# Kernel tuning notes

Measured on AMD Instinct MI355X. Metric: run time of the kernel, lower is better.

## Reference

```python
import jax, jax.numpy as jnp
import numpy as np

D_MODEL = 1024
NUM_HEADS = 16
HEAD_DIM = D_MODEL // NUM_HEADS
BATCH = 4
SEQ = 1024


def setup_inputs() -> dict:
    key = jax.random.key(0)
    ks = jax.random.split(key, 11)
    s = 1.0 / np.sqrt(D_MODEL)
    return {
        "query": jax.random.normal(ks[0], (BATCH, SEQ, D_MODEL), jnp.float32),
        "key_": jax.random.normal(ks[1], (BATCH, SEQ, D_MODEL), jnp.float32),
        "value": jax.random.normal(ks[2], (BATCH, SEQ, D_MODEL), jnp.float32),
        "Wq": jax.random.uniform(ks[3], (D_MODEL, D_MODEL), jnp.float32, -s, s),
        "bq": jax.random.uniform(ks[4], (D_MODEL,), jnp.float32, -s, s),
        "Wk": jax.random.uniform(ks[5], (D_MODEL, D_MODEL), jnp.float32, -s, s),
        "bk": jax.random.uniform(ks[6], (D_MODEL,), jnp.float32, -s, s),
        "Wv": jax.random.uniform(ks[7], (D_MODEL, D_MODEL), jnp.float32, -s, s),
        "bv": jax.random.uniform(ks[8], (D_MODEL,), jnp.float32, -s, s),
        "Wo": jax.random.uniform(ks[9], (D_MODEL, D_MODEL), jnp.float32, -s, s),
        "bo": jax.random.uniform(ks[10], (D_MODEL,), jnp.float32, -s, s),
    }


def reference(query, key_, value, Wq, bq, Wk, bk, Wv, bv, Wo, bo):
    B, S, _ = query.shape
    scale = 1.0 / np.sqrt(HEAD_DIM).astype(np.float32)
    # projections, then split heads: [B, H, S, Dh]
    Q = (query @ Wq.T + bq).reshape(B, S, NUM_HEADS, HEAD_DIM).transpose(0, 2, 1, 3)
    K = (key_ @ Wk.T + bk).reshape(B, S, NUM_HEADS, HEAD_DIM).transpose(0, 2, 1, 3)
    V = (value @ Wv.T + bv).reshape(B, S, NUM_HEADS, HEAD_DIM).transpose(0, 2, 1, 3)
    scores = jnp.einsum("bhqd,bhkd->bhqk", Q, K) * scale
    attention = jax.nn.softmax(scores, axis=-1)
    out = jnp.einsum("bhqk,bhkd->bhqd", attention, V)
    out = out.transpose(0, 2, 1, 3).reshape(B, S, D_MODEL)
    return out @ Wo.T + bo, attention
```

## Files before the change

kernel.cpp:

```cpp
#include <hip/hip_runtime.h>
#include <hip/hip_bf16.h>

#define NH 16
#define S 1024
#define DH 64
#define DM 1024
#define MTOK 4096

typedef __attribute__((ext_vector_type(8))) short bf16x8;
typedef __attribute__((ext_vector_type(4))) float f32x4;
typedef __attribute__((ext_vector_type(16))) float f32x16;
typedef __attribute__((ext_vector_type(8))) unsigned short u16x8;
typedef __attribute__((ext_vector_type(4))) unsigned short u16x4;

__device__ inline unsigned short f2bf(float x) {
  __hip_bfloat16 h = __float2bfloat16(x);
  return __builtin_bit_cast(unsigned short, h);
}

__device__ inline unsigned cvt_pk_bf16(float lo, float hi_) {
  unsigned r;
  asm("v_cvt_pk_bf16_f32 %0, %1, %2" : "=v"(r) : "v"(lo), "v"(hi_));
  return r;
}

__device__ inline void gload16(const void* g, void* lds) {
  __builtin_amdgcn_global_load_lds((const __attribute__((address_space(1))) void*)g,
                                   (__attribute__((address_space(3))) void*)lds, 16, 0, 0);
}

__global__ __launch_bounds__(256) void cvt_all(
    const float* __restrict__ q, const float* __restrict__ k, const float* __restrict__ v,
    const float* __restrict__ wq, const float* __restrict__ wk,
    const float* __restrict__ wv, const float* __restrict__ wo,
    unsigned short* __restrict__ xq, unsigned short* __restrict__ xk,
    unsigned short* __restrict__ xv, unsigned short* __restrict__ wqb,
    unsigned short* __restrict__ wkb, unsigned short* __restrict__ wvb,
    unsigned short* __restrict__ wob) {
  const int bid = blockIdx.x;
  const float* src;
  unsigned short* dst;
  int lb;
  if (bid < 6144) {
    const int r = bid >> 11;
    lb = bid & 2047;
    src = (r == 0) ? q : ((r == 1) ? k : v);
    dst = (r == 0) ? xq : ((r == 1) ? xk : xv);
  } else {
    const int r = (bid - 6144) >> 9;
    lb = (bid - 6144) & 511;
    src = (r == 0) ? wq : ((r == 1) ? wk : ((r == 2) ? wv : wo));
    dst = (r == 0) ? wqb : ((r == 1) ? wkb : ((r == 2) ? wvb : wob));
  }
  const int i = lb * 256 + threadIdx.x;
  const float4* s4 = (const float4*)(src + (size_t)i * 8);
  float4 v0 = s4[0], v1 = s4[1];
  u16x8 o;
  o[0] = f2bf(v0.x); o[1] = f2bf(v0.y); o[2] = f2bf(v0.z); o[3] = f2bf(v0.w);
  o[4] = f2bf(v1.x); o[5] = f2bf(v1.y); o[6] = f2bf(v1.z); o[7] = f2bf(v1.w);
  *(u16x8*)(dst + (size_t)i * 8) = o;
}

__device__ inline void gemm_core128(const unsigned short* __restrict__ X,
                                    const unsigned short* __restrict__ W,
                                    unsigned short* As, unsigned short* Bs,
                                    int m0, int n0, f32x4 acc[4][4]) {
  const int t = threadIdx.x, l = t & 63, w = t >> 6;
  const int wr = w >> 1, wc = w & 1, cl = l & 15, kg = l >> 4;
  const int row0 = w * 16 + (l >> 2);
  const int kcol = (l & 3) * 8;

  const unsigned short* ga0 = X + (size_t)(m0 + row0) * DM + kcol;
  const unsigned short* ga1 = ga0 + (size_t)64 * DM;
  const unsigned short* gb0 = W + (size_t)(n0 + row0) * DM + kcol;
  const unsigned short* gb1 = gb0 + (size_t)64 * DM;
  char* lA0 = (char*)As + w * 1024;
  char* lA1 = (char*)As + w * 1024 + 4096;
  char* lB0 = (char*)Bs + w * 1024;
  char* lB1 = (char*)Bs + w * 1024 + 4096;

  for (int kt = 0; kt < DM; kt += 32) {
    __syncthreads();
    gload16(ga0 + kt, lA0);
    gload16(ga1 + kt, lA1);
    gload16(gb0 + kt, lB0);
    gload16(gb1 + kt, lB1);
    __syncthreads();
    bf16x8 a[4], b[4];
#pragma unroll
    for (int m = 0; m < 4; ++m)
      a[m] = *(const bf16x8*)&As[(wr * 64 + m * 16 + cl) * 32 + kg * 8];
#pragma unroll
    for (int n = 0; n < 4; ++n)
      b[n] = *(const bf16x8*)&Bs[(wc * 64 + n * 16 + cl) * 32 + kg * 8];
#pragma unroll
    for (int m = 0; m < 4; ++m)
#pragma unroll
      for (int n = 0; n < 4; ++n)
        acc[m][n] = __builtin_amdgcn_mfma_f32_16x16x32_bf16(a[m], b[n], acc[m][n], 0, 0, 0);
  }
}

__device__ inline void gemm_core64(const unsigned short* __restrict__ X,
                                   const unsigned short* __restrict__ W,
                                   unsigned short* As, unsigned short* Bs,
                                   int m0, int n0, f32x4 acc[2][4]) {
  const int t = threadIdx.x, l = t & 63, w = t >> 6;
  const int i4 = l >> 2, c8 = (l & 3) * 8;
  const int wr = w >> 1, wc = w & 1, cl = l & 15, kg = l >> 4;

  const unsigned short* ga  = X + (size_t)(m0 + w * 16 + i4) * DM + c8;
  const unsigned short* gb0 = W + (size_t)(n0 + w * 32 + i4) * DM + c8;
  const unsigned short* gb1 = W + (size_t)(n0 + w * 32 + 16 + i4) * DM + c8;
  char* lA  = (char*)As + w * 1024;
  char* lB0 = (char*)Bs + w * 2048;
  char* lB1 = (char*)Bs + w * 2048 + 1024;

  for (int kt = 0; kt < DM; kt += 32) {
    __syncthreads();
    gload16(ga + kt, lA);
    gload16(gb0 + kt, lB0);
    gload16(gb1 + kt, lB1);
    __syncthreads();
    bf16x8 a[2], b[4];
#pragma unroll
    for (int i = 0; i < 2; ++i)
      a[i] = *(const bf16x8*)&As[(wr * 32 + i * 16 + cl) * 32 + kg * 8];
#pragma unroll
    for (int j = 0; j < 4; ++j)
      b[j] = *(const bf16x8*)&Bs[(wc * 64 + j * 16 + cl) * 32 + kg * 8];
#pragma unroll
    for (int i = 0; i < 2; ++i)
#pragma unroll
      for (int j = 0; j < 4; ++j)
        acc[i][j] = __builtin_amdgcn_mfma_f32_16x16x32_bf16(a[i], b[j], acc[i][j], 0, 0, 0);
  }
}

__global__ __launch_bounds__(256) void proj_gemm(
    const unsigned short* __restrict__ X0, const unsigned short* __restrict__ X1,
    const unsigned short* __restrict__ X2, const unsigned short* __restrict__ W0,
    const unsigned short* __restrict__ W1, const unsigned short* __restrict__ W2,
    const float* __restrict__ b0, const float* __restrict__ b1, const float* __restrict__ b2,
    unsigned short* __restrict__ Y0, unsigned short* __restrict__ Y1,
    unsigned short* __restrict__ Y2) {
  __shared__ unsigned short As[128 * 32];
  __shared__ unsigned short Bs[128 * 32];
  const int z = blockIdx.z;
  const unsigned short* X = (z == 0) ? X0 : ((z == 1) ? X1 : X2);
  const unsigned short* W = (z == 0) ? W0 : ((z == 1) ? W1 : W2);
  const float* bias = (z == 0) ? b0 : ((z == 1) ? b1 : b2);
  const int m0 = blockIdx.y * 128, n0 = blockIdx.x * 128;

  f32x4 acc[4][4] = {};
  gemm_core128(X, W, As, Bs, m0, n0, acc);

  const int l = threadIdx.x & 63, w = threadIdx.x >> 6;
  const int wr = w >> 1, wc = w & 1, cl = l & 15, kg = l >> 4;
#pragma unroll
  for (int i = 0; i < 4; ++i) {
#pragma unroll
    for (int j = 0; j < 4; ++j) {
      const int gn = n0 + wc * 64 + j * 16 + cl;
      const float bv = bias[gn];
      const int h_ = gn >> 6, d_ = gn & 63;
      if (z == 2) {
        const int gm0 = m0 + wr * 64 + i * 16 + kg * 4;
        const int b_ = gm0 >> 10, s0 = gm0 & 1023;
        u16x4 vv;
#pragma unroll
        for (int r = 0; r < 4; ++r) vv[r] = f2bf(acc[i][j][r] + bv);
        *(u16x4*)&Y2[((size_t)(b_ * NH + h_) * DH + d_) * S + s0] = vv;
      } else {
#pragma unroll
        for (int r = 0; r < 4; ++r) {
          const int gm = m0 + wr * 64 + i * 16 + kg * 4 + r;
          const int b_ = gm >> 10, s_ = gm & 1023;
          const float val = acc[i][j][r] + bv;
          if (z == 0) {
            Y0[((size_t)(b_ * NH + h_) * S + s_) * DH + d_] = f2bf(val);
          } else {
            Y1[((size_t)(b_ * NH + h_) * S + s_) * DH + d_] = f2bf(val * 0.125f);
          }
        }
      }
    }
  }
}

__global__ __launch_bounds__(256) void out_gemm(const unsigned short* __restrict__ X,
                                                const unsigned short* __restrict__ W,
                                                const float* __restrict__ bias,
                                                float* __restrict__ Y) {
  __shared__ unsigned short As[64 * 32];
  __shared__ unsigned short Bs[128 * 32];
  const int m0 = blockIdx.y * 64, n0 = blockIdx.x * 128;
  f32x4 acc[2][4] = {};
  gemm_core64(X, W, As, Bs, m0, n0, acc);
  const int l = threadIdx.x & 63, w = threadIdx.x >> 6;
  const int wr = w >> 1, wc = w & 1, cl = l & 15, kg = l >> 4;
#pragma unroll
  for (int i = 0; i < 2; ++i) {
#pragma unroll
    for (int j = 0; j < 4; ++j) {
      const int gn = n0 + wc * 64 + j * 16 + cl;
      const float bv = bias[gn];
#pragma unroll
      for (int r = 0; r < 4; ++r) {
        const int gm = m0 + wr * 32 + i * 16 + kg * 4 + r;
        Y[(size_t)gm * DM + gn] = acc[i][j][r] + bv;
      }
    }
  }
}

__global__ __launch_bounds__(512, 4) void attn_mfma(const unsigned short* __restrict__ Qh,
                                                    const unsigned short* __restrict__ Kh,
                                                    const unsigned short* __restrict__ Vt,
                                                    float* __restrict__ attn,
                                                    unsigned short* __restrict__ OutH) {
  __shared__ float sums[8][32];
  __shared__ float Olds[8 * 64 * 33];
  const int t = threadIdx.x, l = t & 63, w = t >> 6;
  const int lq = l & 31, hi = l >> 5;
  const int bh = blockIdx.y;
  const int q0 = blockIdx.x * 32;

  const unsigned short* kb = Kh + (size_t)bh * S * DH;
  const unsigned short* vb = Vt + (size_t)bh * DH * S;

  unsigned e_pk[4][8];
  float sum = 0.f;

  {
    const unsigned short* qp = Qh + ((size_t)bh * S + q0 + lq) * DH + hi * 8;
    bf16x8 qf0 = *(const bf16x8*)(qp);
    bf16x8 qf1 = *(const bf16x8*)(qp + 16);
    bf16x8 qf2 = *(const bf16x8*)(qp + 32);
    bf16x8 qf3 = *(const bf16x8*)(qp + 48);
#pragma unroll
    for (int kt = 0; kt < 4; ++kt) {
      const unsigned short* kp = kb + (size_t)(w * 128 + kt * 32 + lq) * DH + hi * 8;
      f32x16 acc = {};
      __builtin_amdgcn_s_setprio(1);
      acc = __builtin_amdgcn_mfma_f32_32x32x16_bf16(*(const bf16x8*)(kp),      qf0, acc, 0, 0, 0);
      acc = __builtin_amdgcn_mfma_f32_32x32x16_bf16(*(const bf16x8*)(kp + 16), qf1, acc, 0, 0, 0);
      acc = __builtin_amdgcn_mfma_f32_32x32x16_bf16(*(const bf16x8*)(kp + 32), qf2, acc, 0, 0, 0);
      acc = __builtin_amdgcn_mfma_f32_32x32x16_bf16(*(const bf16x8*)(kp + 48), qf3, acc, 0, 0, 0);
      __builtin_amdgcn_s_setprio(0);
      float e[16];
#pragma unroll
      for (int r = 0; r < 16; ++r) e[r] = __expf(acc[r]);
#pragma unroll
      for (int r = 0; r < 16; ++r) sum += e[r];
#pragma unroll
      for (int j = 0; j < 8; ++j) e_pk[kt][j] = cvt_pk_bf16(e[2 * j], e[2 * j + 1]);
    }
  }
  sum += __shfl_xor(sum, 32);
  if (l < 32) sums[w][lq] = sum;
  __syncthreads();
  float tot = 0.f;
#pragma unroll
  for (int p = 0; p < 8; ++p) tot += sums[p][lq];
  const float inv = 1.0f / tot;

  f32x16 o0 = {}, o1 = {};
  float* ab = attn + ((size_t)bh << 20) + ((size_t)(q0 + lq) << 10) + w * 128;

#pragma unroll
  for (int kt = 0; kt < 4; ++kt) {
#pragma unroll
    for (int g = 0; g < 4; ++g) {
      const unsigned pk0 = e_pk[kt][2 * g], pk1 = e_pk[kt][2 * g + 1];
      f32x4 pv;
      pv[0] = __builtin_bit_cast(float, pk0 << 16) * inv;
      pv[1] = __builtin_bit_cast(float, pk0 & 0xffff0000u) * inv;
      pv[2] = __builtin_bit_cast(float, pk1 << 16) * inv;
      pv[3] = __builtin_bit_cast(float, pk1 & 0xffff0000u) * inv;
      *(f32x4*)(ab + kt * 32 + 8 * g + 4 * hi) = pv;
    }

    const unsigned wds0 = e_pk[kt][0], wds1 = e_pk[kt][1];
    const unsigned wds2 = e_pk[kt][2], wds3 = e_pk[kt][3];
    const unsigned wds4 = e_pk[kt][4], wds5 = e_pk[kt][5];
    const unsigned wds6 = e_pk[kt][6], wds7 = e_pk[kt][7];
    const unsigned x0 = __shfl_xor((int)wds0, 32), x1 = __shfl_xor((int)wds1, 32);
    const unsigned x2 = __shfl_xor((int)wds2, 32), x3 = __shfl_xor((int)wds3, 32);
    const unsigned x4 = __shfl_xor((int)wds4, 32), x5 = __shfl_xor((int)wds5, 32);
    const unsigned x6 = __shfl_xor((int)wds6, 32), x7 = __shfl_xor((int)wds7, 32);
    union UU { unsigned u[4]; bf16x8 v; } f0, f1;
    f0.u[0] = hi ? x2 : wds0;  f0.u[1] = hi ? x3 : wds1;
    f0.u[2] = hi ? wds2 : x0;  f0.u[3] = hi ? wds3 : x1;
    f1.u[0] = hi ? x6 : wds4;  f1.u[1] = hi ? x7 : wds5;
    f1.u[2] = hi ? wds6 : x4;  f1.u[3] = hi ? wds7 : x5;

    {
      const unsigned short* vp = vb + (size_t)(lq)*S + w * 128 + kt * 32 + hi * 8;
      bf16x8 v0 = *(const bf16x8*)vp;
      bf16x8 v1 = *(const bf16x8*)(vp + 16);
      const unsigned short* vp1 = vb + (size_t)(32 + lq) * S + w * 128 + kt * 32 + hi * 8;
      bf16x8 v2 = *(const bf16x8*)vp1;
      bf16x8 v3 = *(const bf16x8*)(vp1 + 16);
      __builtin_amdgcn_s_setprio(1);
      o0 = __builtin_amdgcn_mfma_f32_32x32x16_bf16(v0, f0.v, o0, 0, 0, 0);
      o0 = __builtin_amdgcn_mfma_f32_32x32x16_bf16(v1, f1.v, o0, 0, 0, 0);
      o1 = __builtin_amdgcn_mfma_f32_32x32x16_bf16(v2, f0.v, o1, 0, 0, 0);
      o1 = __builtin_amdgcn_mfma_f32_32x32x16_bf16(v3, f1.v, o1, 0, 0, 0);
      __builtin_amdgcn_s_setprio(0);
    }
  }

#pragma unroll
  for (int r = 0; r < 16; ++r) { o0[r] *= inv; o1[r] *= inv; }
#pragma unroll
  for (int g = 0; g < 4; ++g) {
#pragma unroll
    for (int r = 0; r < 4; ++r) {
      const int d = 8 * g + 4 * hi + r;
      Olds[w * 2112 + d * 33 + lq] = o0[4 * g + r];
      Olds[w * 2112 + (32 + d) * 33 + lq] = o1[4 * g + r];
    }
  }
  __syncthreads();

  {
    const int qq = t >> 4, d0 = (t & 15) * 4;
    const int b_ = bh >> 4, h_ = bh & 15;
    u16x4 ov;
#pragma unroll
    for (int i = 0; i < 4; ++i) {
      float s = 0.f;
#pragma unroll
      for (int p = 0; p < 8; ++p) s += Olds[p * 2112 + (d0 + i) * 33 + qq];
      ov[i] = f2bf(s);
    }
    *(u16x4*)&OutH[((size_t)(b_ * S + q0 + qq)) * DM + h_ * DH + d0] = ov;
  }
}

extern "C" void kernel_launch(void* const* d_in, const int* in_sizes, int n_in,
                              void* d_out, int out_size, void* d_ws, size_t ws_size,
                              hipStream_t stream) {
  const float* query = (const float*)d_in[0];
  const float* key_  = (const float*)d_in[1];
  const float* value = (const float*)d_in[2];
  const float* Wq = (const float*)d_in[3];
  const float* bq = (const float*)d_in[4];
  const float* Wk = (const float*)d_in[5];
  const float* bk = (const float*)d_in[6];
  const float* Wv = (const float*)d_in[7];
  const float* bv = (const float*)d_in[8];
  const float* Wo = (const float*)d_in[9];
  const float* bo = (const float*)d_in[10];

  float* out0 = (float*)d_out;
  float* attn = out0 + (size_t)MTOK * DM;

  const size_t M1 = 1u << 20;
  unsigned short* wsu = (unsigned short*)d_ws;
  unsigned short* Xq  = wsu;
  unsigned short* Xk  = wsu + 4 * M1;
  unsigned short* Xv  = wsu + 8 * M1;
  unsigned short* Wqb = wsu + 12 * M1;
  unsigned short* Wkb = wsu + 13 * M1;
  unsigned short* Wvb = wsu + 14 * M1;
  unsigned short* Wob = wsu + 15 * M1;
  unsigned short* Qh  = wsu + 16 * M1;
  unsigned short* Kh  = wsu + 20 * M1;
  unsigned short* Vt  = wsu + 24 * M1;
  unsigned short* OutH= wsu + 28 * M1;

  dim3 tB(256);
  hipLaunchKernelGGL(cvt_all, dim3(8192), tB, 0, stream, query, key_, value, Wq, Wk, Wv, Wo,
                     Xq, Xk, Xv, Wqb, Wkb, Wvb, Wob);

  hipLaunchKernelGGL(proj_gemm, dim3(8, 32, 3), tB, 0, stream,
                     Xq, Xk, Xv, Wqb, Wkb, Wvb, bq, bk, bv, Qh, Kh, Vt);

  hipLaunchKernelGGL(attn_mfma, dim3(32, 64), dim3(512), 0, stream, Qh, Kh, Vt, attn, OutH);

  hipLaunchKernelGGL(out_gemm, dim3(8, 64), tB, 0, stream, OutH, Wob, bo, out0);
}
```

Before: 199.7 us.

## Double GEMM K-tile to 64 and remap blocks for XCD-aware L2 locality

Replaces the two GEMM cores with one templated core that loads a 64-wide K slice per iteration, halving the number of barrier pairs per GEMM at the cost of doubled LDS per block. All three kernels switch to a 1D grid with a swizzled block index so that consecutive blocks dispatched round-robin across the 8 XCDs land on neighbouring tiles, improving L2 reuse of shared K/V and weight rows. The larger LDS footprint may reduce occupancy.

```diff
diff --git a/kernel.cpp b/kernel.cpp
--- a/kernel.cpp
+++ b/kernel.cpp
@@ -61,79 +61,48 @@
   *(u16x8*)(dst + (size_t)i * 8) = o;
 }
 
-__device__ inline void gemm_core128(const unsigned short* __restrict__ X,
-                                    const unsigned short* __restrict__ W,
-                                    unsigned short* As, unsigned short* Bs,
-                                    int m0, int n0, f32x4 acc[4][4]) {
+template <int BM>
+__device__ inline void gemm_core_bk64(const unsigned short* __restrict__ X,
+                                      const unsigned short* __restrict__ W,
+                                      unsigned short* As, unsigned short* Bs,
+                                      int m0, int n0, f32x4 (&acc)[BM / 32][4]) {
+  constexpr int ACH = BM / 32;
   const int t = threadIdx.x, l = t & 63, w = t >> 6;
   const int wr = w >> 1, wc = w & 1, cl = l & 15, kg = l >> 4;
-  const int row0 = w * 16 + (l >> 2);
-  const int kcol = (l & 3) * 8;
-
-  const unsigned short* ga0 = X + (size_t)(m0 + row0) * DM + kcol;
-  const unsigned short* ga1 = ga0 + (size_t)64 * DM;
-  const unsigned short* gb0 = W + (size_t)(n0 + row0) * DM + kcol;
-  const unsigned short* gb1 = gb0 + (size_t)64 * DM;
-  char* lA0 = (char*)As + w * 1024;
-  char* lA1 = (char*)As + w * 1024 + 4096;
-  char* lB0 = (char*)Bs + w * 1024;
-  char* lB1 = (char*)Bs + w * 1024 + 4096;
-
-  for (int kt = 0; kt < DM; kt += 32) {
+  const int lr = l >> 3;
+  const int lc = (l & 7) * 8;
+
+  const unsigned short* gaB = X + (size_t)(m0 + lr) * DM + lc;
+  const unsigned short* gbB = W + (size_t)(n0 + lr) * DM + lc;
+
+  for (int kt = 0; kt < DM; kt += 64) {
     __syncthreads();
-    gload16(ga0 + kt, lA0);
-    gload16(ga1 + kt, lA1);
-    gload16(gb0 + kt, lB0);
-    gload16(gb1 + kt, lB1);
+#pragma unroll
+    for (int c = 0; c < ACH; ++c) {
+      const int ch = w * ACH + c;
+      gload16(gaB + (size_t)(ch * 8) * DM + kt, (char*)As + ch * 1024);
+    }
+#pragma unroll
+    for (int c = 0; c < 4; ++c) {
+      const int ch = w * 4 + c;
+      gload16(gbB + (size_t)(ch * 8) * DM + kt, (char*)Bs + ch * 1024);
+    }
     __syncthreads();
-    bf16x8 a[4], b[4];
-#pragma unroll
-    for (int m = 0; m < 4; ++m)
-      a[m] = *(const bf16x8*)&As[(wr * 64 + m * 16 + cl) * 32 + kg * 8];
-#pragma unroll
-    for (int n = 0; n < 4; ++n)
-      b[n] = *(const bf16x8*)&Bs[(wc * 64 + n * 16 + cl) * 32 + kg * 8];
-#pragma unroll
-    for (int m = 0; m < 4; ++m)
+#pragma unroll
+    for (int kk = 0; kk < 2; ++kk) {
+      bf16x8 a[ACH], b[4];
+#pragma unroll
+      for (int m = 0; m < ACH; ++m)
+        a[m] = *(const bf16x8*)&As[(wr * (BM / 2) + m * 16 + cl) * 64 + kk * 32 + kg * 8];
 #pragma unroll
       for (int n = 0; n < 4; ++n)
-        acc[m][n] = __builtin_amdgcn_mfma_f32_16x16x32_bf16(a[m], b[n], acc[m][n], 0, 0, 0);
-  }
-}
-
-__device__ inline void gemm_core64(const unsigned short* __restrict__ X,
-                                   const unsigned short* __restrict__ W,
-                                   unsigned short* As, unsigned short* Bs,
-                                   int m0, int n0, f32x4 acc[2][4]) {
-  const int t = threadIdx.x, l = t & 63, w = t >> 6;
-  const int i4 = l >> 2, c8 = (l & 3) * 8;
-  const int wr = w >> 1, wc = w & 1, cl = l & 15, kg = l >> 4;
-
-  const unsigned short* ga  = X + (size_t)(m0 + w * 16 + i4) * DM + c8;
-  const unsigned short* gb0 = W + (size_t)(n0 + w * 32 + i4) * DM + c8;
-  const unsigned short* gb1 = W + (size_t)(n0 + w * 32 + 16 + i4) * DM + c8;
-  char* lA  = (char*)As + w * 1024;
-  char* lB0 = (char*)Bs + w * 2048;
-  char* lB1 = (char*)Bs + w * 2048 + 1024;
-
-  for (int kt = 0; kt < DM; kt += 32) {
-    __syncthreads();
-    gload16(ga + kt, lA);
-    gload16(gb0 + kt, lB0);
-    gload16(gb1 + kt, lB1);
-    __syncthreads();
-    bf16x8 a[2], b[4];
-#pragma unroll
-    for (int i = 0; i < 2; ++i)
-      a[i] = *(const bf16x8*)&As[(wr * 32 + i * 16 + cl) * 32 + kg * 8];
-#pragma unroll
-    for (int j = 0; j < 4; ++j)
-      b[j] = *(const bf16x8*)&Bs[(wc * 64 + j * 16 + cl) * 32 + kg * 8];
-#pragma unroll
-    for (int i = 0; i < 2; ++i)
-#pragma unroll
-      for (int j = 0; j < 4; ++j)
-        acc[i][j] = __builtin_amdgcn_mfma_f32_16x16x32_bf16(a[i], b[j], acc[i][j], 0, 0, 0);
+        b[n] = *(const bf16x8*)&Bs[(wc * 64 + n * 16 + cl) * 64 + kk * 32 + kg * 8];
+#pragma unroll
+      for (int m = 0; m < ACH; ++m)
+#pragma unroll
+        for (int n = 0; n < 4; ++n)
+          acc[m][n] = __builtin_amdgcn_mfma_f32_16x16x32_bf16(a[m], b[n], acc[m][n], 0, 0, 0);
+    }
   }
 }
 
@@ -144,16 +113,20 @@
     const float* __restrict__ b0, const float* __restrict__ b1, const float* __restrict__ b2,
     unsigned short* __restrict__ Y0, unsigned short* __restrict__ Y1,
     unsigned short* __restrict__ Y2) {
-  __shared__ unsigned short As[128 * 32];
-  __shared__ unsigned short Bs[128 * 32];
-  const int z = blockIdx.z;
+  __shared__ unsigned short As[128 * 64];
+  __shared__ unsigned short Bs[128 * 64];
+  const int bid = blockIdx.x;
+  const int wg = (bid & 7) * 96 + (bid >> 3);
+  const int z = wg >> 8;
+  const int rem = wg & 255;
+  const int m0 = (rem >> 3) * 128, n0 = (rem & 7) * 128;
+
   const unsigned short* X = (z == 0) ? X0 : ((z == 1) ? X1 : X2);
   const unsigned short* W = (z == 0) ? W0 : ((z == 1) ? W1 : W2);
   const float* bias = (z == 0) ? b0 : ((z == 1) ? b1 : b2);
-  const int m0 = blockIdx.y * 128, n0 = blockIdx.x * 128;
 
   f32x4 acc[4][4] = {};
-  gemm_core128(X, W, As, Bs, m0, n0, acc);
+  gemm_core_bk64<128>(X, W, As, Bs, m0, n0, acc);
 
   const int l = threadIdx.x & 63, w = threadIdx.x >> 6;
   const int wr = w >> 1, wc = w & 1, cl = l & 15, kg = l >> 4;
@@ -192,11 +165,15 @@
                                                 const unsigned short* __restrict__ W,
                                                 const float* __restrict__ bias,
                                                 float* __restrict__ Y) {
-  __shared__ unsigned short As[64 * 32];
-  __shared__ unsigned short Bs[128 * 32];
-  const int m0 = blockIdx.y * 64, n0 = blockIdx.x * 128;
+  __shared__ unsigned short As[64 * 64];
+  __shared__ unsigned short Bs[128 * 64];
+  const int bid = blockIdx.x;
+  const int wg = (bid & 7) * 64 + (bid >> 3);
+  const int m0 = (wg >> 3) * 64, n0 = (wg & 7) * 128;
+
   f32x4 acc[2][4] = {};
-  gemm_core64(X, W, As, Bs, m0, n0, acc);
+  gemm_core_bk64<64>(X, W, As, Bs, m0, n0, acc);
+
   const int l = threadIdx.x & 63, w = threadIdx.x >> 6;
   const int wr = w >> 1, wc = w & 1, cl = l & 15, kg = l >> 4;
 #pragma unroll
@@ -223,8 +200,10 @@
   __shared__ float Olds[8 * 64 * 33];
   const int t = threadIdx.x, l = t & 63, w = t >> 6;
   const int lq = l & 31, hi = l >> 5;
-  const int bh = blockIdx.y;
-  const int q0 = blockIdx.x * 32;
+  const int bid = blockIdx.x;
+  const int wg = (bid & 7) * 256 + (bid >> 3);
+  const int bh = wg >> 5;
+  const int q0 = (wg & 31) * 32;
 
   const unsigned short* kb = Kh + (size_t)bh * S * DH;
   const unsigned short* vb = Vt + (size_t)bh * DH * S;
@@ -375,10 +354,10 @@
   hipLaunchKernelGGL(cvt_all, dim3(8192), tB, 0, stream, query, key_, value, Wq, Wk, Wv, Wo,
                      Xq, Xk, Xv, Wqb, Wkb, Wvb, Wob);
 
-  hipLaunchKernelGGL(proj_gemm, dim3(8, 32, 3), tB, 0, stream,
+  hipLaunchKernelGGL(proj_gemm, dim3(768), tB, 0, stream,
                      Xq, Xk, Xv, Wqb, Wkb, Wvb, bq, bk, bv, Qh, Kh, Vt);
 
-  hipLaunchKernelGGL(attn_mfma, dim3(32, 64), dim3(512), 0, stream, Qh, Kh, Vt, attn, OutH);
-
-  hipLaunchKernelGGL(out_gemm, dim3(8, 64), tB, 0, stream, OutH, Wob, bo, out0);
-}
+  hipLaunchKernelGGL(attn_mfma, dim3(2048), dim3(512), 0, stream, Qh, Kh, Vt, attn, OutH);
+
+  hipLaunchKernelGGL(out_gemm, dim3(512), tB, 0, stream, OutH, Wob, bo, out0);
+}
```

New measurement: 200.0 us. No clear change (+0.1%).
